# Kernel tuning notes

Measured on AMD Instinct MI355X. Metric: run time of the kernel, lower is better.

The kernel has to match this reference:

```python
import jax, jax.numpy as jnp
import numpy as np

B, N, D, H = 4, 2048, 512, 8
HD = D // H


def setup_inputs() -> dict:
    key = jax.random.key(0)
    ks = jax.random.split(key, 12)
    s = 1.0 / np.sqrt(D)
    return {
        "node_feat": jax.random.normal(ks[0], (B, N, D), jnp.float32),
        "edge_weights": jax.random.uniform(ks[1], (B, N, N), jnp.float32),
        "adj_matrix": jax.random.uniform(ks[2], (B, N, N), jnp.float32),
        "masks": jnp.ones((B, N), jnp.float32),
        "class_token": 0.02 * jax.random.normal(ks[3], (1, 1, D), jnp.float32),
        "Wq": jax.random.uniform(ks[4], (D, D), jnp.float32, -s, s),
        "bq": jnp.zeros((D,), jnp.float32),
        "Wk": jax.random.uniform(ks[5], (D, D), jnp.float32, -s, s),
        "bk": jnp.zeros((D,), jnp.float32),
        "Wv": jax.random.uniform(ks[6], (D, D), jnp.float32, -s, s),
        "bv": jnp.zeros((D,), jnp.float32),
        "Wo": jax.random.uniform(ks[7], (D, D), jnp.float32, -s, s),
        "bo": jnp.zeros((D,), jnp.float32),
        "gamma": jnp.ones((D,), jnp.float32),
        "beta": jnp.zeros((D,), jnp.float32),
    }


def _attn_mask(edge_weights, masks):
    # inner block: edge gates + self-loops, clamped at 1
    inner = jnp.minimum(edge_weights + jnp.eye(N, dtype=edge_weights.dtype), 1.0)
    top = jnp.concatenate([jnp.ones((B, 1, 1), edge_weights.dtype), masks[:, None, :]], axis=2)  # [B,1,1+N]
    bot = jnp.concatenate([jnp.ones((B, N, 1), edge_weights.dtype), inner], axis=2)              # [B,N,1+N]
    m = jnp.concatenate([top, bot], axis=1)  # [B,1+N,1+N]
    ext = jnp.concatenate([jnp.ones((B, 1), masks.dtype), masks], axis=1)  # [B,1+N], CLS always valid
    return m * ext[:, None, :] * ext[:, :, None]


def reference(node_feat, edge_weights, adj_matrix, masks, class_token,
              Wq, bq, Wk, bk, Wv, bv, Wo, bo, gamma, beta):
    x = jnp.concatenate([jnp.broadcast_to(class_token, (B, 1, D)), node_feat], axis=1)  # [B,1+N,D]
    S = 1 + N
    q = (x @ Wq.T + bq).reshape(B, S, H, HD).transpose(0, 2, 1, 3)
    k = (x @ Wk.T + bk).reshape(B, S, H, HD).transpose(0, 2, 1, 3)
    v = (x @ Wv.T + bv).reshape(B, S, H, HD).transpose(0, 2, 1, 3)
    scores = jnp.einsum('bhqd,bhkd->bhqk', q, k) / jnp.sqrt(jnp.float32(HD))
    m = _attn_mask(edge_weights, masks)
    scores = jnp.where(m[:, None, :, :] == 0, jnp.float32(-1e9), scores)
    attn = jax.nn.softmax(scores, axis=-1)
    out = jnp.einsum('bhqk,bhkd->bhqd', attn, v).transpose(0, 2, 1, 3).reshape(B, S, D)
    out = out @ Wo.T + bo
    y = out + x
    mu = jnp.mean(y, axis=-1, keepdims=True)
    var = jnp.mean((y - mu) ** 2, axis=-1, keepdims=True)
    y = (y - mu) / jnp.sqrt(var + 1e-5) * gamma + beta
    return y[:, 0, :]
```

## Files before the change

kernel.cpp:

```cpp
#include <hip/hip_runtime.h>

#define B_ 4
#define N_ 2048
#define D_ 512
#define H_ 8
#define S_ (N_ + 1)
#define SC 16
#define NCH 129
#define NBLK (NCH * B_)

#define TQ_OFF   64
#define W2_OFF   8192
#define Z_OFF    (W2_OFF + B_ * H_ * D_)

__device__ __forceinline__ float wave_reduce_sum(float v) {
    #pragma unroll
    for (int off = 32; off > 0; off >>= 1) v += __shfl_down(v, off, 64);
    return v;
}
__device__ __forceinline__ float wave_allreduce_sum(float v) {
    #pragma unroll
    for (int off = 1; off < 64; off <<= 1) v += __shfl_xor(v, off, 64);
    return v;
}
__device__ __forceinline__ float dot8(float4 a, float4 b, float4 c, float4 d) {
    return a.x*b.x + a.y*b.y + a.z*b.z + a.w*b.w
         + c.x*d.x + c.y*d.y + c.z*d.z + c.w*d.w;
}

__global__ void __launch_bounds__(512)
setup_kernel(const float* __restrict__ nf, const float* __restrict__ ct,
             const float* __restrict__ Wq, const float* __restrict__ bq,
             const float* __restrict__ Wk,
             const float* __restrict__ Wv, const float* __restrict__ Wo,
             float* __restrict__ ws) {
    __shared__ float q0s[64];
    __shared__ float part[4][128];
    const int blk = blockIdx.x;
    const int tid = threadIdx.x, wv = tid >> 6, lane = tid & 63;

    if (blk < 32) {
        const int h = blk >> 2, jq = blk & 3;
        const float4* c4 = (const float4*)ct;
        float4 ca = c4[lane * 2], cb = c4[lane * 2 + 1];
        #pragma unroll
        for (int i = 0; i < 8; ++i) {
            int rl = wv + 8 * i;
            int r  = h * 64 + rl;
            const float4* row = (const float4*)(Wq + (size_t)r * D_);
            float4 a = row[lane * 2], b = row[lane * 2 + 1];
            float acc = dot8(a, ca, b, cb);
            acc = wave_reduce_sum(acc);
            if (lane == 0) q0s[rl] = acc + bq[r];
        }
        __syncthreads();
        {
            int jj = tid & 127, g = tid >> 7;
            int j  = jq * 128 + jj;
            float acc = 0.f;
            #pragma unroll
            for (int d = 0; d < 16; ++d) {
                int d2 = g * 16 + d;
                acc += q0s[d2] * Wk[(size_t)(h * 64 + d2) * D_ + j];
            }
            part[g][jj] = acc;
        }
        __syncthreads();
        if (tid < 128)
            ws[TQ_OFF + h * D_ + jq * 128 + tid] =
                part[0][tid] + part[1][tid] + part[2][tid] + part[3][tid];
        return;
    }

    if (blk < 64)          ws[W2_OFF + (size_t)(blk - 32) * 512 + tid] = 0.f;
    else if (blk == 64) {  if (tid < B_ * H_) ws[Z_OFF + tid] = 0.f; }

    {
        int chunk = blk >> 2, b4 = blk & 3;
        int s0 = chunk * SC;
        float sink = 0.f;
        #pragma unroll
        for (int i = 0; i < 2; ++i) {
            int s = s0 + wv * 2 + i;
            if (s >= 1 && s <= N_) {
                const float4* x4 = (const float4*)(nf + ((size_t)b4 * N_ + (s - 1)) * D_);
                float4 xa = x4[lane], xb = x4[64 + lane];
                sink += xa.x + xb.w;
            }
        }
        int r = blk & 511;
        const float4* rv = (const float4*)(Wv + (size_t)r * D_);
        const float4* ro = (const float4*)(Wo + (size_t)r * D_);
        sink += rv[lane * 2].x + rv[lane * 2 + 1].w + ro[lane * 2].x + ro[lane * 2 + 1].w;
        asm volatile("" :: "v"(sink));
    }
}

__global__ void __launch_bounds__(512)
scores_wsum_kernel(const float* __restrict__ nf, const float* __restrict__ ct,
                   const float* __restrict__ masks, float* __restrict__ ws) {
    __shared__ float sa[H_ * SC];
    const int blk = blockIdx.x;
    const int tid = threadIdx.x, wv = tid >> 6, lane = tid & 63;
    const int chunk = blk >> 2, b4 = blk & 3;
    const int s0 = chunk * SC;

    {
        const float4* t4 = (const float4*)(ws + TQ_OFF);
        #pragma unroll
        for (int i = 0; i < 2; ++i) {
            int ss = wv + 8 * i;
            int s  = s0 + ss;
            if (s < S_) {
                const float* xrow = (s == 0) ? ct : (nf + ((size_t)b4 * N_ + (s - 1)) * D_);
                const float4* x4 = (const float4*)xrow;
                float4 xa = x4[lane], xb = x4[64 + lane];
                float gate = 1.0f;
                if (s > 0) gate = (masks[b4 * N_ + s - 1] != 0.0f) ? 1.0f : 0.0f;
                float p[H_];
                #pragma unroll
                for (int h = 0; h < H_; ++h) {
                    float4 ta = t4[h * 128 + lane], tb = t4[h * 128 + 64 + lane];
                    p[h] = dot8(ta, xa, tb, xb);
                    p[h] = wave_allreduce_sum(p[h]);
                }
                if (lane == 0) {
                    #pragma unroll
                    for (int h = 0; h < H_; ++h)
                        sa[(h << 4) + ss] = gate * __expf(p[h] * 0.125f);
                }
            } else if (lane == 0) {
                #pragma unroll
                for (int h = 0; h < H_; ++h) sa[(h << 4) + ss] = 0.f;
            }
        }
    }
    __syncthreads();
    {
        float acc[H_];
        #pragma unroll
        for (int h = 0; h < H_; ++h) acc[h] = 0.f;
        int smax = min(SC, S_ - s0);
        for (int ss = 0; ss < smax; ++ss) {
            int s = s0 + ss;
            const float* xrow = (s == 0) ? ct : (nf + ((size_t)b4 * N_ + (s - 1)) * D_);
            float xv = xrow[tid];
            #pragma unroll
            for (int h = 0; h < H_; ++h) acc[h] += sa[(h << 4) + ss] * xv;
        }
        #pragma unroll
        for (int h = 0; h < H_; ++h)
            atomicAdd(ws + W2_OFF + (size_t)(b4 * H_ + h) * D_ + tid, acc[h]);
        if (tid < H_) {
            float z = 0.f;
            #pragma unroll
            for (int ss = 0; ss < SC; ++ss) z += sa[(tid << 4) + ss];
            atomicAdd(ws + Z_OFF + b4 * H_ + tid, z);
        }
    }
}

__global__ void __launch_bounds__(1024)
tail_kernel(const float* __restrict__ Wv, const float* __restrict__ bv,
            const float* __restrict__ Wo, const float* __restrict__ bo,
            const float* __restrict__ ct,
            const float* __restrict__ gamma, const float* __restrict__ beta,
            const float* __restrict__ ws, float* __restrict__ out) {
    __shared__ float o0s[512];
    __shared__ float ys[512];
    __shared__ float r1[8], r2[8];
    const int b = blockIdx.x;
    const int tid = threadIdx.x, wv = tid >> 6, lane = tid & 63;

    {
        const int head = wv >> 1;
        const float4* wr = (const float4*)(ws + W2_OFF + (size_t)(b * H_ + head) * D_);
        float4 wa = wr[lane * 2], wb = wr[lane * 2 + 1];
        float zi = 1.0f / ws[Z_OFF + b * H_ + head];
        for (int i = 0; i < 32; ++i) {
            int r = wv * 32 + i;
            const float4* row = (const float4*)(Wv + (size_t)r * D_);
            float4 a = row[lane * 2], c = row[lane * 2 + 1];
            float acc = dot8(a, wa, c, wb);
            acc = wave_reduce_sum(acc);
            if (lane == 0) o0s[r] = acc * zi + bv[r];
        }
    }
    __syncthreads();
    {
        const float4* ov = (const float4*)o0s;
        float4 oa = ov[lane * 2], ob = ov[lane * 2 + 1];
        for (int i = 0; i < 32; ++i) {
            int r = wv * 32 + i;
            const float4* row = (const float4*)(Wo + (size_t)r * D_);
            float4 a = row[lane * 2], c = row[lane * 2 + 1];
            float acc = dot8(a, oa, c, ob);
            acc = wave_reduce_sum(acc);
            if (lane == 0) ys[r] = acc + bo[r] + ct[r];
        }
    }
    __syncthreads();
    if (tid < 512) {
        float v = ys[tid];
        float s1 = v, s2 = v * v;
        #pragma unroll
        for (int off = 32; off > 0; off >>= 1) {
            s1 += __shfl_down(s1, off, 64);
            s2 += __shfl_down(s2, off, 64);
        }
        if (lane == 0) { r1[wv] = s1; r2[wv] = s2; }
    }
    __syncthreads();
    if (tid == 0) {
        float a = 0.f, c = 0.f;
        for (int i = 0; i < 8; ++i) { a += r1[i]; c += r2[i]; }
        r1[0] = a; r2[0] = c;
    }
    __syncthreads();
    if (tid < 512) {
        float v = ys[tid];
        float mean = r1[0] * (1.0f / D_);
        float var  = r2[0] * (1.0f / D_) - mean * mean;
        float rinv = rsqrtf(var + 1e-5f);
        out[b * D_ + tid] = (v - mean) * rinv * gamma[tid] + beta[tid];
    }
}

extern "C" void kernel_launch(void* const* d_in, const int* in_sizes, int n_in,
                              void* d_out, int out_size, void* d_ws, size_t ws_size,
                              hipStream_t stream) {
    const float* nf    = (const float*)d_in[0];
    const float* masks = (const float*)d_in[3];
    const float* ct    = (const float*)d_in[4];
    const float* Wq    = (const float*)d_in[5];
    const float* bq    = (const float*)d_in[6];
    const float* Wk    = (const float*)d_in[7];
    const float* Wv    = (const float*)d_in[9];
    const float* bv    = (const float*)d_in[10];
    const float* Wo    = (const float*)d_in[11];
    const float* bo    = (const float*)d_in[12];
    const float* gamma = (const float*)d_in[13];
    const float* beta  = (const float*)d_in[14];
    float* ws  = (float*)d_ws;
    float* out = (float*)d_out;

    hipLaunchKernelGGL(setup_kernel,       dim3(NBLK), dim3(512),  0, stream,
                       nf, ct, Wq, bq, Wk, Wv, Wo, ws);
    hipLaunchKernelGGL(scores_wsum_kernel, dim3(NBLK), dim3(512),  0, stream,
                       nf, ct, masks, ws);
    hipLaunchKernelGGL(tail_kernel,        dim3(B_),   dim3(1024), 0, stream,
                       Wv, bv, Wo, bo, ct, gamma, beta, ws, out);
}
```

Before: 226.9 us.

## Split tail matvecs across many blocks with last-block LayerNorm via atomic ticket

Replaces the 4-block tail kernel, in which each block ran both 512x512 matvecs serially, with two 256-block kernels. The first computes the Wv projection of the weighted sum; the second computes the Wo projection and uses a per-batch atomic ticket so the last finishing block does the LayerNorm. The aim is to spread the tail's weight reads over many CUs instead of four. In exchange it adds one kernel launch, workspace round-trips for the intermediates, and counter zeroing in setup.

After: 187.2 us. -17.5%, faster.

```diff
diff --git a/kernel.cpp b/kernel.cpp
--- a/kernel.cpp
+++ b/kernel.cpp
@@ -12,6 +12,9 @@
 #define TQ_OFF   64
 #define W2_OFF   8192
 #define Z_OFF    (W2_OFF + B_ * H_ * D_)
+#define CNT_OFF  (Z_OFF + 32)
+#define O0_OFF   (CNT_OFF + 32)
+#define Y_OFF    (O0_OFF + B_ * D_)
 
 __device__ __forceinline__ float wave_reduce_sum(float v) {
     #pragma unroll
@@ -73,7 +76,7 @@
     }
 
     if (blk < 64)          ws[W2_OFF + (size_t)(blk - 32) * 512 + tid] = 0.f;
-    else if (blk == 64) {  if (tid < B_ * H_) ws[Z_OFF + tid] = 0.f; }
+    else if (blk == 64) {  if (tid < 36) ws[Z_OFF + tid] = 0.f; }
 
     {
         int chunk = blk >> 2, b4 = blk & 3;
@@ -160,48 +163,54 @@
     }
 }
 
-__global__ void __launch_bounds__(1024)
-tail_kernel(const float* __restrict__ Wv, const float* __restrict__ bv,
-            const float* __restrict__ Wo, const float* __restrict__ bo,
-            const float* __restrict__ ct,
-            const float* __restrict__ gamma, const float* __restrict__ beta,
-            const float* __restrict__ ws, float* __restrict__ out) {
-    __shared__ float o0s[512];
-    __shared__ float ys[512];
+__global__ void __launch_bounds__(512)
+wv_kernel(const float* __restrict__ Wv, const float* __restrict__ bv,
+          float* __restrict__ ws) {
+    const int blk = blockIdx.x;
+    const int b = blk >> 6, g = blk & 63;
+    const int wv = threadIdx.x >> 6, lane = threadIdx.x & 63;
+    const int head = g >> 3;
+    const int r = g * 8 + wv;
+    const float4* wr = (const float4*)(ws + W2_OFF + (size_t)(b * H_ + head) * D_);
+    float4 wa = wr[lane * 2], wb = wr[lane * 2 + 1];
+    float zi = 1.0f / ws[Z_OFF + b * H_ + head];
+    const float4* row = (const float4*)(Wv + (size_t)r * D_);
+    float4 a = row[lane * 2], c = row[lane * 2 + 1];
+    float acc = dot8(a, wa, c, wb);
+    acc = wave_reduce_sum(acc);
+    if (lane == 0) ws[O0_OFF + b * D_ + r] = acc * zi + bv[r];
+}
+
+__global__ void __launch_bounds__(512)
+wo_ln_kernel(const float* __restrict__ Wo, const float* __restrict__ bo,
+             const float* __restrict__ ct,
+             const float* __restrict__ gamma, const float* __restrict__ beta,
+             float* __restrict__ ws, float* __restrict__ out) {
     __shared__ float r1[8], r2[8];
-    const int b = blockIdx.x;
+    __shared__ unsigned ticket;
+    const int blk = blockIdx.x;
+    const int b = blk >> 6, g = blk & 63;
     const int tid = threadIdx.x, wv = tid >> 6, lane = tid & 63;
 
     {
-        const int head = wv >> 1;
-        const float4* wr = (const float4*)(ws + W2_OFF + (size_t)(b * H_ + head) * D_);
-        float4 wa = wr[lane * 2], wb = wr[lane * 2 + 1];
-        float zi = 1.0f / ws[Z_OFF + b * H_ + head];
-        for (int i = 0; i < 32; ++i) {
-            int r = wv * 32 + i;
-            const float4* row = (const float4*)(Wv + (size_t)r * D_);
-            float4 a = row[lane * 2], c = row[lane * 2 + 1];
-            float acc = dot8(a, wa, c, wb);
-            acc = wave_reduce_sum(acc);
-            if (lane == 0) o0s[r] = acc * zi + bv[r];
-        }
+        int r = g * 8 + wv;
+        const float4* ov = (const float4*)(ws + O0_OFF + (size_t)b * D_);
+        float4 oa = ov[lane * 2], ob = ov[lane * 2 + 1];
+        const float4* row = (const float4*)(Wo + (size_t)r * D_);
+        float4 a = row[lane * 2], c = row[lane * 2 + 1];
+        float acc = dot8(a, oa, c, ob);
+        acc = wave_reduce_sum(acc);
+        if (lane == 0) ws[Y_OFF + b * D_ + r] = acc + bo[r] + ct[r];
     }
     __syncthreads();
-    {
-        const float4* ov = (const float4*)o0s;
-        float4 oa = ov[lane * 2], ob = ov[lane * 2 + 1];
-        for (int i = 0; i < 32; ++i) {
-            int r = wv * 32 + i;
-            const float4* row = (const float4*)(Wo + (size_t)r * D_);
-            float4 a = row[lane * 2], c = row[lane * 2 + 1];
-            float acc = dot8(a, oa, c, ob);
-            acc = wave_reduce_sum(acc);
-            if (lane == 0) ys[r] = acc + bo[r] + ct[r];
-        }
-    }
+    if (tid == 0)
+        ticket = __hip_atomic_fetch_add((unsigned*)ws + CNT_OFF + b, 1u,
+                                        __ATOMIC_ACQ_REL, __HIP_MEMORY_SCOPE_AGENT);
     __syncthreads();
-    if (tid < 512) {
-        float v = ys[tid];
+    if (ticket != 63) return;
+
+    {
+        float v = ws[Y_OFF + b * D_ + tid];
         float s1 = v, s2 = v * v;
         #pragma unroll
         for (int off = 32; off > 0; off >>= 1) {
@@ -209,16 +218,13 @@
             s2 += __shfl_down(s2, off, 64);
         }
         if (lane == 0) { r1[wv] = s1; r2[wv] = s2; }
-    }
-    __syncthreads();
-    if (tid == 0) {
-        float a = 0.f, c = 0.f;
-        for (int i = 0; i < 8; ++i) { a += r1[i]; c += r2[i]; }
-        r1[0] = a; r2[0] = c;
-    }
-    __syncthreads();
-    if (tid < 512) {
-        float v = ys[tid];
+        __syncthreads();
+        if (tid == 0) {
+            float a = 0.f, c = 0.f;
+            for (int i = 0; i < 8; ++i) { a += r1[i]; c += r2[i]; }
+            r1[0] = a; r2[0] = c;
+        }
+        __syncthreads();
         float mean = r1[0] * (1.0f / D_);
         float var  = r2[0] * (1.0f / D_) - mean * mean;
         float rinv = rsqrtf(var + 1e-5f);
@@ -244,10 +250,12 @@
     float* ws  = (float*)d_ws;
     float* out = (float*)d_out;
 
-    hipLaunchKernelGGL(setup_kernel,       dim3(NBLK), dim3(512),  0, stream,
+    hipLaunchKernelGGL(setup_kernel,       dim3(NBLK), dim3(512), 0, stream,
                        nf, ct, Wq, bq, Wk, Wv, Wo, ws);
-    hipLaunchKernelGGL(scores_wsum_kernel, dim3(NBLK), dim3(512),  0, stream,
+    hipLaunchKernelGGL(scores_wsum_kernel, dim3(NBLK), dim3(512), 0, stream,
                        nf, ct, masks, ws);
-    hipLaunchKernelGGL(tail_kernel,        dim3(B_),   dim3(1024), 0, stream,
-                       Wv, bv, Wo, bo, ct, gamma, beta, ws, out);
-}
+    hipLaunchKernelGGL(wv_kernel,          dim3(256),  dim3(512), 0, stream,
+                       Wv, bv, ws);
+    hipLaunchKernelGGL(wo_ln_kernel,       dim3(256),  dim3(512), 0, stream,
+                       Wo, bo, ct, gamma, beta, ws, out);
+}
```
